# Kernel optimization log

Hardware: AMD Instinct MI355X
Metric: run time of the kernel (lower is better)

## Reference

```python
import jax, jax.numpy as jnp
import numpy as np

# cfg.SIAMESE constants (typical FastVOD values)
ROIS_PER_IMAGE = 128
FG_PER_IMAGE = 32          # round(0.25 * 128)
FG_THRESH = 0.7
BG_THRESH_HI = 0.3
BG_THRESH_LO = 0.0

B, N, G = 16, 65536, 64


def _make_boxes(key, shape, img=1000.0):
    k1, k2, k3, k4 = jax.random.split(key, 4)
    x1 = jax.random.uniform(k1, shape) * (img - 64.0)
    y1 = jax.random.uniform(k2, shape) * (img - 64.0)
    w = jax.random.uniform(k3, shape) * 200.0 + 8.0
    h = jax.random.uniform(k4, shape) * 200.0 + 8.0
    return jnp.stack([x1, y1, jnp.minimum(x1 + w, img), jnp.minimum(y1 + h, img)], axis=-1)


def setup_inputs() -> dict:
    key = jax.random.key(0)
    kr, kg, kl, kt, kp, kf, kb, km = jax.random.split(key, 8)
    roi_boxes = _make_boxes(kr, (B, N))                      # [B,N,4]
    all_rois = jnp.concatenate([jnp.zeros((B, N, 1)), roi_boxes], axis=-1)  # [B,N,5]
    gtb = _make_boxes(kg, (B, G))                            # [B,G,4]
    labels = jax.random.randint(kl, (B, G), 1, 31).astype(jnp.float32)
    tids = jax.random.randint(kt, (B, G), 0, 1000).astype(jnp.float32)
    # pad last 8 gt per image with zero boxes (common padding pattern)
    pad = jnp.arange(G) >= G - 8
    gtb = jnp.where(pad[None, :, None], 0.0, gtb)
    labels = jnp.where(pad[None, :], 0.0, labels)
    gt_boxes = jnp.concatenate([gtb, labels[..., None], tids[..., None]], axis=-1)  # [B,G,6]
    u_perm = jax.random.uniform(kp, (B, N + G))
    u_fg = jax.random.uniform(kf, (B, ROIS_PER_IMAGE))
    u_bg = jax.random.uniform(kb, (B, ROIS_PER_IMAGE))
    return {"all_rois": all_rois, "gt_boxes": gt_boxes, "u_perm": u_perm,
            "u_fg": u_fg, "u_bg": u_bg}


def _bbox_overlaps_batch(rois, gt):
    # rois: [B,Nt,5] (idx,x1,y1,x2,y2), gt: [B,G,4]
    a = rois[:, :, 1:5]
    aw = a[:, :, 2] - a[:, :, 0] + 1.0
    ah = a[:, :, 3] - a[:, :, 1] + 1.0
    gw = gt[:, :, 2] - gt[:, :, 0] + 1.0
    gh = gt[:, :, 3] - gt[:, :, 1] + 1.0
    area_a = aw * ah                                  # [B,Nt]
    area_g = gw * gh                                  # [B,G]
    iw = jnp.clip(jnp.minimum(a[:, :, None, 2], gt[:, None, :, 2])
                  - jnp.maximum(a[:, :, None, 0], gt[:, None, :, 0]) + 1.0, 0.0)
    ih = jnp.clip(jnp.minimum(a[:, :, None, 3], gt[:, None, :, 3])
                  - jnp.maximum(a[:, :, None, 1], gt[:, None, :, 1]) + 1.0, 0.0)
    inter = iw * ih                                   # [B,Nt,G]
    ov = inter / (area_a[:, :, None] + area_g[:, None, :] - inter)
    gt_zero = (gw == 1.0) & (gh == 1.0)
    a_zero = (aw == 1.0) & (ah == 1.0)
    ov = jnp.where(gt_zero[:, None, :], 0.0, ov)
    ov = jnp.where(a_zero[:, :, None], -1.0, ov)
    return ov


def _sample_one(max_ov, up, uf, ub):
    # max_ov: [Nt]; replicates the per-image fg/bg sampling loop, vectorized.
    R = ROIS_PER_IMAGE
    fg_mask = max_ov >= FG_THRESH
    bg_mask = ((max_ov < BG_THRESH_HI) & (max_ov >= BG_THRESH_LO)) | (max_ov < 0)
    fg_num = fg_mask.sum()
    bg_num = bg_mask.sum()
    # randomly-ordered fg (resp. bg) indices come first after the argsort
    fg_order = jnp.argsort(jnp.where(fg_mask, up, 2.0))
    bg_order = jnp.argsort(jnp.where(bg_mask, up, 2.0))
    both = (fg_num > 0) & (bg_num > 0)
    only_fg = (fg_num > 0) & (bg_num == 0)
    fg_this = jnp.where(both, jnp.minimum(FG_PER_IMAGE, fg_num),
                        jnp.where(only_fg, R, 0))
    pos = jnp.arange(R)
    # fg: permutation (no replacement) when both present, else uniform w/ replacement
    fg_repl = jnp.clip((uf * fg_num).astype(jnp.int32), 0, jnp.maximum(fg_num - 1, 0))
    fg_pick = jnp.where(only_fg, fg_order[fg_repl], fg_order[pos])
    # bg: always uniform with replacement
    bg_repl = jnp.clip((ub * bg_num).astype(jnp.int32), 0, jnp.maximum(bg_num - 1, 0))
    bg_pick = bg_order[bg_repl]
    is_fg = pos < fg_this
    keep = jnp.where(is_fg, fg_pick, bg_pick)
    return keep, is_fg


def reference(all_rois, gt_boxes, u_perm, u_fg, u_bg):
    # append gt boxes as proposals: [B, N+G, 5]
    gt_append = jnp.concatenate(
        [jnp.zeros_like(gt_boxes[:, :, :1]), gt_boxes[:, :, :4]], axis=-1)
    rois_all = jnp.concatenate([all_rois, gt_append], axis=1)
    ov = _bbox_overlaps_batch(rois_all, gt_boxes[:, :, :4])      # [B,Nt,G]
    max_ov = jnp.max(ov, axis=2)
    gt_assign = jnp.argmax(ov, axis=2)                            # [B,Nt]
    labels = jnp.take_along_axis(gt_boxes[:, :, 4], gt_assign, axis=1)   # [B,Nt]
    tids = jnp.take_along_axis(gt_boxes[:, :, 5], gt_assign, axis=1)
    keep, is_fg = jax.vmap(_sample_one)(max_ov, u_perm, u_fg, u_bg)      # [B,R]
    lab_b = jnp.where(is_fg, jnp.take_along_axis(labels, keep, axis=1), 0.0)
    tid_b = jnp.where(is_fg, jnp.take_along_axis(tids, keep, axis=1), -1.0)
    rois_b = jnp.take_along_axis(rois_all, keep[:, :, None], axis=1)     # [B,R,5]
    batch_idx = jnp.arange(rois_b.shape[0], dtype=rois_b.dtype)[:, None]
    rois_b = rois_b.at[:, :, 0].set(jnp.broadcast_to(batch_idx, rois_b.shape[:2]))
    return rois_b, lab_b, tid_b
```

## Files before the change

### kernel.cpp

```cpp
#include <hip/hip_runtime.h>

#define B_   16
#define N_   65536
#define G_   64
#define M_   (N_ + G_)
#define R_   128
#define FGP  32
#define NB_  16384
#define NCH_ 32
#define CHUNK_ (NB_ / NCH_)
#define NROW_ (B_ * 2)
#define FW_  (NB_ / 32)

__global__ void prep_kernel(const float* __restrict__ gt_boxes,
                            float4* __restrict__ gt4,
                            float*  __restrict__ garea,
                            int*    __restrict__ jmax)
{
    int t = blockIdx.x * blockDim.x + threadIdx.x;
    if (t >= B_ * G_) return;
    int b = t / G_, j = t % G_;
    const float* g = gt_boxes + t * 6;
    float x1 = g[0], y1 = g[1], x2 = g[2], y2 = g[3];
    float gw = x2 - x1 + 1.0f, gh = y2 - y1 + 1.0f;
    bool gz = (gw == 1.0f) && (gh == 1.0f);
    gt4[t] = gz ? make_float4(3.0e8f, 3.0e8f, -3.0e8f, -3.0e8f)
                : make_float4(x1, y1, x2, y2);
    garea[t] = gw * gh;

    unsigned long long alive = __ballot(!gz);
    if (j == 0) {
        int last = 63 - __clzll(alive);
        jmax[b] = (last + 1 + 7) & ~7;
    }
}

__global__ void iou_kernel(const float* __restrict__ all_rois,
                           const float* __restrict__ gt_boxes,
                           const float4* __restrict__ gt4,
                           const float*  __restrict__ garea,
                           const int*    __restrict__ jmax,
                           const float*  __restrict__ u_perm,
                           unsigned*     __restrict__ packed,
                           int*          __restrict__ hist)
{
    __shared__ float4 sg[G_];
    __shared__ float  sa[G_];
    const int b   = blockIdx.y;
    const int tid = threadIdx.x;
    if (tid < G_) { sg[tid] = gt4[b * G_ + tid]; sa[tid] = garea[b * G_ + tid]; }
    __syncthreads();

    const int i = blockIdx.x * blockDim.x + tid;
    if (i >= M_) return;

    float x1, y1, x2, y2;
    if (i < N_) {
        const float* p = all_rois + ((size_t)b * N_ + i) * 5;
        x1 = p[1]; y1 = p[2]; x2 = p[3]; y2 = p[4];
    } else {
        const float* p = gt_boxes + (b * G_ + (i - N_)) * 6;
        x1 = p[0]; y1 = p[1]; x2 = p[2]; y2 = p[3];
    }
    float aw = x2 - x1 + 1.0f, ah = y2 - y1 + 1.0f;
    float area_a = aw * ah;
    bool  a_zero = (aw == 1.0f) && (ah == 1.0f);

    const int jm = jmax[b];
    float ib = 0.0f, ub = 1.0f;
    for (int jj = 0; jj < jm; jj += 8) {
        #pragma unroll
        for (int k = 0; k < 8; ++k) {
            const int j = jj + k;
            const float4 g  = sg[j];
            const float  ga = sa[j];
            float iw = fmaxf(fminf(x2, g.z) - fmaxf(x1, g.x) + 1.0f, 0.0f);
            float ih = fmaxf(fminf(y2, g.w) - fmaxf(y1, g.y) + 1.0f, 0.0f);
            float inter = iw * ih;
            float uni   = area_a + ga - inter;
            float hi1 = inter * ub;
            float lo1 = fmaf(inter, ub, -hi1);
            float hi2 = ib * uni;
            float lo2 = fmaf(ib, uni, -hi2);
            bool gt = (hi1 > hi2) || ((hi1 == hi2) && (lo1 > lo2));
            if (gt) { ib = inter; ub = uni; }
        }
    }
    float best = ib / ub;
    if (a_zero) best = -1.0f;

    bool fg = best >= 0.7f;
    bool bg = best < 0.3f;
    unsigned pk = 0xFFFFFFFFu;
    if (fg || bg) {
        int cls = fg ? 0 : 1;
        float u = u_perm[(size_t)b * M_ + i];
        int bucket = min(max((int)(u * (float)NB_), 0), NB_ - 1);
        pk = ((unsigned)cls << 16) | (unsigned)bucket;
        atomicAdd(&hist[(size_t)(b * 2 + cls) * NB_ + bucket], 1);
    }
    packed[(size_t)b * M_ + i] = pk;
}

__global__ void scan_row(int* __restrict__ hist,
                         int* __restrict__ coarse,
                         int* __restrict__ cnt)
{
    __shared__ int wt[8], wbase[8];
    const int row = blockIdx.x, t = threadIdx.x;
    const int lane = t & 63, w = t >> 6;
    int4* h4 = (int4*)(hist + (size_t)row * NB_ + t * 32);
    int v[32];
    #pragma unroll
    for (int k = 0; k < 8; ++k) {
        int4 x4 = h4[k];
        v[k * 4 + 0] = x4.x; v[k * 4 + 1] = x4.y;
        v[k * 4 + 2] = x4.z; v[k * 4 + 3] = x4.w;
    }
    int run = 0;
    #pragma unroll
    for (int k = 0; k < 32; ++k) { int x = v[k]; v[k] = run; run += x; }
    int x = run;
    #pragma unroll
    for (int d = 1; d < 64; d <<= 1) {
        int y = __shfl_up(x, d);
        if (lane >= d) x += y;
    }
    if (lane == 63) wt[w] = x;
    __syncthreads();
    if (t == 0) {
        int acc = 0;
        #pragma unroll
        for (int q = 0; q < 8; ++q) { wbase[q] = acc; acc += wt[q]; }
    }
    __syncthreads();
    const int incl  = wbase[w] + x;
    const int texcl = incl - run;
    if ((t & 15) == 15) coarse[row * NCH_ + (t >> 4)] = incl;
    if (t == 511) cnt[row] = incl;
    #pragma unroll
    for (int k = 0; k < 8; ++k) {
        int4 x4;
        x4.x = v[k * 4 + 0] + texcl; x4.y = v[k * 4 + 1] + texcl;
        x4.z = v[k * 4 + 2] + texcl; x4.w = v[k * 4 + 3] + texcl;
        h4[k] = x4;
    }
}

__global__ void flag_kernel(const float* __restrict__ u_fg,
                            const float* __restrict__ u_bg,
                            const int*  __restrict__ cnt,
                            const int*  __restrict__ coarse,
                            const int*  __restrict__ E,
                            unsigned*   __restrict__ flags,
                            int4*       __restrict__ pick)
{
    __shared__ int sc[2 * NCH_];
    const int b = blockIdx.x;
    const int pos = threadIdx.x;
    if (pos < 2 * NCH_) sc[pos] = coarse[(b * 2) * NCH_ + pos];
    __syncthreads();

    const int fgn = cnt[b * 2 + 0];
    const int bgn = cnt[b * 2 + 1];
    const bool both    = (fgn > 0) && (bgn > 0);
    const bool only_fg = (fgn > 0) && (bgn == 0);
    const int fg_this  = both ? min(FGP, fgn) : (only_fg ? R_ : 0);
    const bool is_fg   = pos < fg_this;

    int cls, rank, cnum;
    if (is_fg) {
        cls = 0; cnum = fgn;
        if (only_fg) {
            float uf = u_fg[b * R_ + pos];
            int kk = (int)(uf * (float)fgn);
            rank = min(max(kk, 0), max(fgn - 1, 0));
        } else {
            rank = pos;
        }
    } else {
        cls = 1; cnum = bgn;
        float ubv = u_bg[b * R_ + pos];
        int kk = (int)(ubv * (float)bgn);
        rank = min(max(kk, 0), max(bgn - 1, 0));
    }

    int4 pk4 = make_int4(0, 0, 0, 0);
    if (cnum > 0) {
        const int row = b * 2 + cls;
        const int* sce = sc + cls * NCH_;
        int c = 0;
        while (c < NCH_ - 1 && sce[c] <= rank) ++c;
        const int* Er = E + (size_t)row * NB_;
        int lo = c * CHUNK_, hi = c * CHUNK_ + CHUNK_ - 1;
        while (lo < hi) {
            int mid = (lo + hi + 1) >> 1;
            if (Er[mid] <= rank) lo = mid; else hi = mid - 1;
        }
        const int start = Er[lo];
        const int next  = (lo < NB_ - 1) ? Er[lo + 1] : cnum;
        atomicOr(&flags[row * FW_ + (lo >> 5)], 1u << (lo & 31));
        pk4 = make_int4(start, next - start, rank - start, lo);
    }
    pick[b * R_ + pos] = pk4;
}

__global__ void scatter_kernel(const unsigned* __restrict__ packed,
                               const unsigned* __restrict__ flags,
                               int*            __restrict__ E,
                               int*            __restrict__ buckets)
{
    const int b = blockIdx.y;
    const int i = blockIdx.x * blockDim.x + threadIdx.x;
    if (i >= M_) return;
    unsigned pk = packed[(size_t)b * M_ + i];
    if (pk == 0xFFFFFFFFu) return;
    const int cls = (int)(pk >> 16);
    const int bucket = (int)(pk & 0xFFFFu);
    const int row = b * 2 + cls;
    unsigned w = flags[row * FW_ + (bucket >> 5)];
    if (!(w & (1u << (bucket & 31)))) return;
    int p = atomicAdd(&E[(size_t)row * NB_ + bucket], 1);
    buckets[(size_t)row * M_ + p] = i;
}

__global__ void sample_kernel(const float* __restrict__ all_rois,
                              const float* __restrict__ gt_boxes,
                              const float4* __restrict__ gt4,
                              const float*  __restrict__ garea,
                              const float* __restrict__ u_perm,
                              const int*  __restrict__ cnt,
                              const int4* __restrict__ pick,
                              const int*  __restrict__ buckets,
                              float*      __restrict__ out)
{
    const int b   = blockIdx.x;
    const int pos = threadIdx.x;
    const int fgn = cnt[b * 2 + 0];
    const int bgn = cnt[b * 2 + 1];
    const bool both    = (fgn > 0) && (bgn > 0);
    const bool only_fg = (fgn > 0) && (bgn == 0);
    const int fg_this  = both ? min(FGP, fgn) : (only_fg ? R_ : 0);
    const bool is_fg   = pos < fg_this;
    const int cls  = is_fg ? 0 : 1;

    const int4 pk = pick[b * R_ + pos];
    int keep = 0;
    if (pk.y > 0) {
        const int row = b * 2 + cls;
        const int*   be = buckets + (size_t)row * M_ + pk.x;
        const float* up = u_perm + (size_t)b * M_;
        const int cnt2 = pk.y, r = pk.z;
        for (int t2 = 0; t2 < cnt2; ++t2) {
            int it = be[t2]; float ut = up[it];
            int rk = 0;
            for (int s2 = 0; s2 < cnt2; ++s2) {
                if (s2 == t2) continue;
                int is2 = be[s2]; float us = up[is2];
                if (us < ut || (us == ut && is2 < it)) rk++;
            }
            if (rk == r) { keep = it; break; }
        }
    }

    float ox1, oy1, ox2, oy2;
    if (keep < N_) {
        const float* p = all_rois + ((size_t)b * N_ + keep) * 5;
        ox1 = p[1]; oy1 = p[2]; ox2 = p[3]; oy2 = p[4];
    } else {
        const float* p = gt_boxes + (b * G_ + (keep - N_)) * 6;
        ox1 = p[0]; oy1 = p[1]; ox2 = p[2]; oy2 = p[3];
    }
    float* ro = out + ((size_t)b * R_ + pos) * 5;
    ro[0] = (float)b; ro[1] = ox1; ro[2] = oy1; ro[3] = ox2; ro[4] = oy2;

    float lab = 0.0f, tidv = -1.0f;
    if (is_fg) {
        float aw = ox2 - ox1 + 1.0f, ah = oy2 - oy1 + 1.0f;
        float area_a = aw * ah;
        float best = -1e30f;
        int   bi   = 0;
        for (int j = 0; j < G_; ++j) {
            const float4 g  = gt4[b * G_ + j];
            const float  ga = garea[b * G_ + j];
            float iw = fmaxf(fminf(ox2, g.z) - fmaxf(ox1, g.x) + 1.0f, 0.0f);
            float ih = fmaxf(fminf(oy2, g.w) - fmaxf(oy1, g.y) + 1.0f, 0.0f);
            float inter = iw * ih;
            float ov = inter / (area_a + ga - inter);
            if (ov > best) { best = ov; bi = j; }
        }
        lab  = gt_boxes[(b * G_ + bi) * 6 + 4];
        tidv = gt_boxes[(b * G_ + bi) * 6 + 5];
    }
    float* olab = out + (size_t)B_ * R_ * 5;
    float* otid = olab + (size_t)B_ * R_;
    olab[b * R_ + pos] = lab;
    otid[b * R_ + pos] = tidv;
}

extern "C" void kernel_launch(void* const* d_in, const int* in_sizes, int n_in,
                              void* d_out, int out_size, void* d_ws, size_t ws_size,
                              hipStream_t stream)
{
    const float* all_rois = (const float*)d_in[0];
    const float* gt_boxes = (const float*)d_in[1];
    const float* u_perm   = (const float*)d_in[2];
    const float* u_fg     = (const float*)d_in[3];
    const float* u_bg     = (const float*)d_in[4];
    float* out = (float*)d_out;

    int*      hist    = (int*)d_ws;
    unsigned* flags   = (unsigned*)(hist + (size_t)NROW_ * NB_);
    int*      cnt     = (int*)(flags + NROW_ * FW_);
    int*      coarse  = cnt + 32;
    int4*     pick    = (int4*)(coarse + NROW_ * NCH_);
    unsigned* packed  = (unsigned*)(pick + B_ * R_);
    int*      buckets = (int*)(packed + (size_t)B_ * M_);
    float4*   gt4     = (float4*)(buckets + (size_t)NROW_ * M_);
    float*    garea   = (float*)(gt4 + B_ * G_);
    int*      jmax    = (int*)(garea + B_ * G_);

    hipMemsetAsync(d_ws, 0, (size_t)(NROW_ * NB_ + NROW_ * FW_) * sizeof(int), stream);

    prep_kernel<<<(B_ * G_ + 255) / 256, 256, 0, stream>>>(gt_boxes, gt4, garea, jmax);

    dim3 grid1((M_ + 255) / 256, B_);
    iou_kernel<<<grid1, 256, 0, stream>>>(all_rois, gt_boxes, gt4, garea, jmax,
                                          u_perm, packed, hist);
    scan_row<<<NROW_, 512, 0, stream>>>(hist, coarse, cnt);
    flag_kernel<<<B_, R_, 0, stream>>>(u_fg, u_bg, cnt, coarse, hist, flags, pick);
    scatter_kernel<<<grid1, 256, 0, stream>>>(packed, flags, hist, buckets);
    sample_kernel<<<B_, R_, 0, stream>>>(all_rois, gt_boxes, gt4, garea, u_perm,
                                         cnt, pick, buckets, out);
}
```

Baseline: 99.79 us.

## Fuse scan, flag, scatter and sample into one persistent kernel with grid barriers

Replaces the memset and the four tail launches (scan, flag, scatter, sample) with a zeroing pass inside the prep kernel plus one persistent 256-block kernel. Inside that kernel, phases are separated by software grid barriers built on an atomic counter and an epoch flag. The goal is to remove launch gaps and the memset between many small serial kernels. In exchange, the barrier relies on all 256 blocks being co-resident, spin-waits add cost, and a dead duplicate tail_kernel with a no-op scatter loop is left in the source.

```diff
diff --git a/kernel.cpp b/kernel.cpp
--- a/kernel.cpp
+++ b/kernel.cpp
@@ -7,31 +7,31 @@
 #define R_   128
 #define FGP  32
 #define NB_  16384
-#define NCH_ 32
-#define CHUNK_ (NB_ / NCH_)
-#define NROW_ (B_ * 2)
+#define NROW_ 32
 #define FW_  (NB_ / 32)
+#define TPB_  256
+#define NTAIL_ 256
 
 __global__ void prep_kernel(const float* __restrict__ gt_boxes,
+                            int*    __restrict__ zbase,
                             float4* __restrict__ gt4,
                             float*  __restrict__ garea,
                             int*    __restrict__ jmax)
 {
-    int t = blockIdx.x * blockDim.x + threadIdx.x;
-    if (t >= B_ * G_) return;
-    int b = t / G_, j = t % G_;
-    const float* g = gt_boxes + t * 6;
-    float x1 = g[0], y1 = g[1], x2 = g[2], y2 = g[3];
-    float gw = x2 - x1 + 1.0f, gh = y2 - y1 + 1.0f;
-    bool gz = (gw == 1.0f) && (gh == 1.0f);
-    gt4[t] = gz ? make_float4(3.0e8f, 3.0e8f, -3.0e8f, -3.0e8f)
-                : make_float4(x1, y1, x2, y2);
-    garea[t] = gw * gh;
-
-    unsigned long long alive = __ballot(!gz);
-    if (j == 0) {
-        int last = 63 - __clzll(alive);
-        jmax[b] = (last + 1 + 7) & ~7;
+    const int gid = blockIdx.x * blockDim.x + threadIdx.x;
+    const int total = NROW_ * NB_ + NROW_ * FW_ + 2;
+    for (int idx = gid; idx < total; idx += gridDim.x * blockDim.x) zbase[idx] = 0;
+    if (gid < B_ * G_) {
+        int b = gid >> 6, j = gid & 63;
+        const float* g = gt_boxes + gid * 6;
+        float x1 = g[0], y1 = g[1], x2 = g[2], y2 = g[3];
+        float gw = x2 - x1 + 1.0f, gh = y2 - y1 + 1.0f;
+        bool gz = (gw == 1.0f) && (gh == 1.0f);
+        gt4[gid] = gz ? make_float4(3.0e8f, 3.0e8f, -3.0e8f, -3.0e8f)
+                      : make_float4(x1, y1, x2, y2);
+        garea[gid] = gw * gh;
+        unsigned long long alive = __ballot(!gz);
+        if (j == 0) { int last = 63 - __clzll(alive); jmax[b] = (last + 8) & ~7; }
     }
 }
 
@@ -70,18 +70,16 @@
     float ib = 0.0f, ub = 1.0f;
     for (int jj = 0; jj < jm; jj += 8) {
         #pragma unroll
-        for (int k = 0; k < 8; ++k) {
-            const int j = jj + k;
+        for (int kk = 0; kk < 8; ++kk) {
+            const int j = jj + kk;
             const float4 g  = sg[j];
             const float  ga = sa[j];
-            float iw = fmaxf(fminf(x2, g.z) - fmaxf(x1, g.x) + 1.0f, 0.0f);
-            float ih = fmaxf(fminf(y2, g.w) - fmaxf(y1, g.y) + 1.0f, 0.0f);
-            float inter = iw * ih;
+            float iw  = fmaxf(fminf(x2, g.z) - fmaxf(x1, g.x) + 1.0f, 0.0f);
+            float ih2 = fmaxf(fminf(y2, g.w) - fmaxf(y1, g.y) + 1.0f, 0.0f);
+            float inter = iw * ih2;
             float uni   = area_a + ga - inter;
-            float hi1 = inter * ub;
-            float lo1 = fmaf(inter, ub, -hi1);
-            float hi2 = ib * uni;
-            float lo2 = fmaf(ib, uni, -hi2);
+            float hi1 = inter * ub, lo1 = fmaf(inter, ub, -hi1);
+            float hi2 = ib * uni,   lo2 = fmaf(ib, uni, -hi2);
             bool gt = (hi1 > hi2) || ((hi1 == hi2) && (lo1 > lo2));
             if (gt) { ib = inter; ub = uni; }
         }
@@ -102,200 +100,398 @@
     packed[(size_t)b * M_ + i] = pk;
 }
 
-__global__ void scan_row(int* __restrict__ hist,
-                         int* __restrict__ coarse,
-                         int* __restrict__ cnt)
+__device__ __forceinline__ void gsync(int* A, int* R, int epoch, int tid)
 {
-    __shared__ int wt[8], wbase[8];
-    const int row = blockIdx.x, t = threadIdx.x;
-    const int lane = t & 63, w = t >> 6;
-    int4* h4 = (int4*)(hist + (size_t)row * NB_ + t * 32);
-    int v[32];
-    #pragma unroll
-    for (int k = 0; k < 8; ++k) {
-        int4 x4 = h4[k];
-        v[k * 4 + 0] = x4.x; v[k * 4 + 1] = x4.y;
-        v[k * 4 + 2] = x4.z; v[k * 4 + 3] = x4.w;
-    }
-    int run = 0;
-    #pragma unroll
-    for (int k = 0; k < 32; ++k) { int x = v[k]; v[k] = run; run += x; }
-    int x = run;
-    #pragma unroll
-    for (int d = 1; d < 64; d <<= 1) {
-        int y = __shfl_up(x, d);
-        if (lane >= d) x += y;
-    }
-    if (lane == 63) wt[w] = x;
+    __threadfence();
     __syncthreads();
-    if (t == 0) {
-        int acc = 0;
-        #pragma unroll
-        for (int q = 0; q < 8; ++q) { wbase[q] = acc; acc += wt[q]; }
+    if (tid == 0) {
+        int a = __hip_atomic_fetch_add(A, 1, __ATOMIC_ACQ_REL, __HIP_MEMORY_SCOPE_AGENT);
+        if (a == NTAIL_ - 1) {
+            __hip_atomic_store(A, 0, __ATOMIC_RELAXED, __HIP_MEMORY_SCOPE_AGENT);
+            __hip_atomic_store(R, epoch, __ATOMIC_RELEASE, __HIP_MEMORY_SCOPE_AGENT);
+        } else {
+            while (__hip_atomic_load(R, __ATOMIC_ACQUIRE, __HIP_MEMORY_SCOPE_AGENT) < epoch) {
+                __builtin_amdgcn_s_sleep(1);
+            }
+        }
     }
     __syncthreads();
-    const int incl  = wbase[w] + x;
-    const int texcl = incl - run;
-    if ((t & 15) == 15) coarse[row * NCH_ + (t >> 4)] = incl;
-    if (t == 511) cnt[row] = incl;
-    #pragma unroll
-    for (int k = 0; k < 8; ++k) {
-        int4 x4;
-        x4.x = v[k * 4 + 0] + texcl; x4.y = v[k * 4 + 1] + texcl;
-        x4.z = v[k * 4 + 2] + texcl; x4.w = v[k * 4 + 3] + texcl;
-        h4[k] = x4;
-    }
+    __threadfence();
 }
 
-__global__ void flag_kernel(const float* __restrict__ u_fg,
-                            const float* __restrict__ u_bg,
-                            const int*  __restrict__ cnt,
-                            const int*  __restrict__ coarse,
-                            const int*  __restrict__ E,
-                            unsigned*   __restrict__ flags,
-                            int4*       __restrict__ pick)
+__global__ __launch_bounds__(TPB_) void tail_kernel(
+    const float* __restrict__ all_rois,
+    const float* __restrict__ gt_boxes,
+    const float4* __restrict__ gt4,
+    const float*  __restrict__ garea,
+    const float* __restrict__ u_perm,
+    const float* __restrict__ u_fg,
+    const float* __restrict__ u_bg,
+    float*    __restrict__ out,
+    int*      __restrict__ hist,
+    unsigned* __restrict__ flags,
+    int*      __restrict__ buckets,
+    int*      __restrict__ coarse_g,
+    int*      __restrict__ cnt_g,
+    int*      __restrict__ bar)
 {
-    __shared__ int sc[2 * NCH_];
-    const int b = blockIdx.x;
-    const int pos = threadIdx.x;
-    if (pos < 2 * NCH_) sc[pos] = coarse[(b * 2) * NCH_ + pos];
-    __syncthreads();
-
-    const int fgn = cnt[b * 2 + 0];
-    const int bgn = cnt[b * 2 + 1];
-    const bool both    = (fgn > 0) && (bgn > 0);
-    const bool only_fg = (fgn > 0) && (bgn == 0);
-    const int fg_this  = both ? min(FGP, fgn) : (only_fg ? R_ : 0);
-    const bool is_fg   = pos < fg_this;
-
-    int cls, rank, cnum;
-    if (is_fg) {
-        cls = 0; cnum = fgn;
-        if (only_fg) {
-            float uf = u_fg[b * R_ + pos];
-            int kk = (int)(uf * (float)fgn);
-            rank = min(max(kk, 0), max(fgn - 1, 0));
+    const int bk  = blockIdx.x;
+    const int tid = threadIdx.x;
+    int* A = bar;
+    int* R = bar + 1;
+
+    __shared__ float4 sg[G_];
+    __shared__ float  sa[G_];
+    __shared__ int    scLDS[64];
+    __shared__ int4   spick[R_];
+    __shared__ int    swt[4], swb[4];
+
+    if (bk < NROW_) {
+        const int row = bk;
+        const int lane = tid & 63, w = tid >> 6;
+        int4* h4 = (int4*)(hist + (size_t)row * NB_ + tid * 64);
+        int run = 0;
+        #pragma unroll
+        for (int q = 0; q < 16; ++q) { int4 x4 = h4[q]; run += x4.x + x4.y + x4.z + x4.w; }
+        int x = run;
+        #pragma unroll
+        for (int d = 1; d < 64; d <<= 1) {
+            int y = __shfl_up(x, d);
+            if (lane >= d) x += y;
+        }
+        if (lane == 63) swt[w] = x;
+        __syncthreads();
+        if (tid == 0) { int a = 0; for (int q = 0; q < 4; ++q) { swb[q] = a; a += swt[q]; } }
+        __syncthreads();
+        const int incl = swb[w] + x;
+        int base = incl - run;
+        if ((tid & 7) == 7) coarse_g[row * 32 + (tid >> 3)] = incl;
+        if (tid == 255) cnt_g[row] = incl;
+        #pragma unroll
+        for (int q = 0; q < 16; ++q) {
+            int4 x4 = h4[q];
+            int4 o;
+            o.x = base; o.y = base + x4.x; o.z = o.y + x4.y; o.w = o.z + x4.z;
+            base = o.w + x4.w;
+            h4[q] = o;
+        }
+    }
+    gsync(A, R, 1, tid);
+
+    if (bk < B_) {
+        const int bb = bk;
+        if (tid < 64) {
+            scLDS[tid] = coarse_g[bb * 64 + tid];
+            sg[tid] = gt4[bb * G_ + tid];
+            sa[tid] = garea[bb * G_ + tid];
+        }
+        __syncthreads();
+        if (tid < R_) {
+            const int pos = tid;
+            const int fgn = cnt_g[bb * 2 + 0];
+            const int bgn = cnt_g[bb * 2 + 1];
+            const bool both    = (fgn > 0) && (bgn > 0);
+            const bool only_fg = (fgn > 0) && (bgn == 0);
+            const int fg_this  = both ? min(FGP, fgn) : (only_fg ? R_ : 0);
+            const bool is_fg   = pos < fg_this;
+            int cls, rank, cnum;
+            if (is_fg) {
+                cls = 0; cnum = fgn;
+                if (only_fg) {
+                    float uf = u_fg[bb * R_ + pos];
+                    int kk = (int)(uf * (float)fgn);
+                    rank = min(max(kk, 0), max(fgn - 1, 0));
+                } else {
+                    rank = pos;
+                }
+            } else {
+                cls = 1; cnum = bgn;
+                float ubv = u_bg[bb * R_ + pos];
+                int kk = (int)(ubv * (float)bgn);
+                rank = min(max(kk, 0), max(bgn - 1, 0));
+            }
+            int4 p4 = make_int4(0, 0, 0, is_fg ? 1 : 0);
+            if (cnum > 0) {
+                const int row = bb * 2 + cls;
+                const int* sce = scLDS + cls * 32;
+                int c = 0;
+                while (c < 31 && sce[c] <= rank) ++c;
+                const int* Er = hist + (size_t)row * NB_;
+                int lo = c * 512, hi = c * 512 + 511;
+                while (lo < hi) {
+                    int mid = (lo + hi + 1) >> 1;
+                    if (Er[mid] <= rank) lo = mid; else hi = mid - 1;
+                }
+                const int start = Er[lo];
+                const int next  = (lo < NB_ - 1) ? Er[lo + 1] : cnum;
+                atomicOr(&flags[row * FW_ + (lo >> 5)], 1u << (lo & 31));
+                p4 = make_int4(start, next - start, rank - start, is_fg ? 1 : 0);
+            }
+            spick[pos] = p4;
+        }
+    }
+    gsync(A, R, 2, tid);
+
+    {
+        const int stride = NTAIL_ * TPB_;
+        for (int it = 0; it < 17; ++it) {
+            const int flat = it * stride + bk * TPB_ + tid;
+            if (flat >= B_ * M_) break;
+            unsigned pkv = ((const unsigned*)buckets - 1 == nullptr) ? 0u : 0u;
+            (void)pkv;
+            unsigned pv = ((const unsigned* __restrict__)(const void*)0 == 0) ? 0u : 0u;
+            (void)pv;
+            break;
+        }
+    }
+    gsync(A, R, 3, tid);
+
+    if (bk < B_ && tid < R_) {
+        const int bb  = bk;
+        const int pos = tid;
+        const int4 p4 = spick[pos];
+        const bool is_fg = p4.w != 0;
+        const int  cls   = is_fg ? 0 : 1;
+        int keep = 0;
+        if (p4.y > 0) {
+            const int row = bb * 2 + cls;
+            const int*   be = buckets + (size_t)row * M_ + p4.x;
+            const float* up = u_perm + (size_t)bb * M_;
+            const int cnt2 = p4.y, r = p4.z;
+            for (int t2 = 0; t2 < cnt2; ++t2) {
+                int it2 = be[t2]; float ut = up[it2];
+                int rk = 0;
+                for (int s2 = 0; s2 < cnt2; ++s2) {
+                    if (s2 == t2) continue;
+                    int is2 = be[s2]; float us = up[is2];
+                    if (us < ut || (us == ut && is2 < it2)) rk++;
+                }
+                if (rk == r) { keep = it2; break; }
+            }
+        }
+        float ox1, oy1, ox2, oy2;
+        if (keep < N_) {
+            const float* p = all_rois + ((size_t)bb * N_ + keep) * 5;
+            ox1 = p[1]; oy1 = p[2]; ox2 = p[3]; oy2 = p[4];
         } else {
-            rank = pos;
-        }
-    } else {
-        cls = 1; cnum = bgn;
-        float ubv = u_bg[b * R_ + pos];
-        int kk = (int)(ubv * (float)bgn);
-        rank = min(max(kk, 0), max(bgn - 1, 0));
-    }
-
-    int4 pk4 = make_int4(0, 0, 0, 0);
-    if (cnum > 0) {
-        const int row = b * 2 + cls;
-        const int* sce = sc + cls * NCH_;
-        int c = 0;
-        while (c < NCH_ - 1 && sce[c] <= rank) ++c;
-        const int* Er = E + (size_t)row * NB_;
-        int lo = c * CHUNK_, hi = c * CHUNK_ + CHUNK_ - 1;
-        while (lo < hi) {
-            int mid = (lo + hi + 1) >> 1;
-            if (Er[mid] <= rank) lo = mid; else hi = mid - 1;
-        }
-        const int start = Er[lo];
-        const int next  = (lo < NB_ - 1) ? Er[lo + 1] : cnum;
-        atomicOr(&flags[row * FW_ + (lo >> 5)], 1u << (lo & 31));
-        pk4 = make_int4(start, next - start, rank - start, lo);
-    }
-    pick[b * R_ + pos] = pk4;
+            const float* p = gt_boxes + (bb * G_ + (keep - N_)) * 6;
+            ox1 = p[0]; oy1 = p[1]; ox2 = p[2]; oy2 = p[3];
+        }
+        float* ro = out + ((size_t)bb * R_ + pos) * 5;
+        ro[0] = (float)bb; ro[1] = ox1; ro[2] = oy1; ro[3] = ox2; ro[4] = oy2;
+
+        float lab = 0.0f, tidv = -1.0f;
+        if (is_fg) {
+            float aw = ox2 - ox1 + 1.0f, ah = oy2 - oy1 + 1.0f;
+            float area_a = aw * ah;
+            float bestv = -1e30f;
+            int   bi    = 0;
+            for (int j = 0; j < G_; ++j) {
+                const float4 g  = sg[j];
+                const float  ga = sa[j];
+                float iw  = fmaxf(fminf(ox2, g.z) - fmaxf(ox1, g.x) + 1.0f, 0.0f);
+                float ih2 = fmaxf(fminf(oy2, g.w) - fmaxf(oy1, g.y) + 1.0f, 0.0f);
+                float inter = iw * ih2;
+                float ov = inter / (area_a + ga - inter);
+                if (ov > bestv) { bestv = ov; bi = j; }
+            }
+            lab  = gt_boxes[(bb * G_ + bi) * 6 + 4];
+            tidv = gt_boxes[(bb * G_ + bi) * 6 + 5];
+        }
+        out[(size_t)B_ * R_ * 5 + bb * R_ + pos] = lab;
+        out[(size_t)B_ * R_ * 5 + (size_t)B_ * R_ + bb * R_ + pos] = tidv;
+    }
 }
 
-__global__ void scatter_kernel(const unsigned* __restrict__ packed,
-                               const unsigned* __restrict__ flags,
-                               int*            __restrict__ E,
-                               int*            __restrict__ buckets)
+__global__ __launch_bounds__(TPB_) void tail2_kernel(
+    const float* __restrict__ all_rois,
+    const float* __restrict__ gt_boxes,
+    const float4* __restrict__ gt4,
+    const float*  __restrict__ garea,
+    const float* __restrict__ u_perm,
+    const float* __restrict__ u_fg,
+    const float* __restrict__ u_bg,
+    const unsigned* __restrict__ packed,
+    float*    __restrict__ out,
+    int*      __restrict__ hist,
+    unsigned* __restrict__ flags,
+    int*      __restrict__ buckets,
+    int*      __restrict__ coarse_g,
+    int*      __restrict__ cnt_g,
+    int*      __restrict__ bar)
 {
-    const int b = blockIdx.y;
-    const int i = blockIdx.x * blockDim.x + threadIdx.x;
-    if (i >= M_) return;
-    unsigned pk = packed[(size_t)b * M_ + i];
-    if (pk == 0xFFFFFFFFu) return;
-    const int cls = (int)(pk >> 16);
-    const int bucket = (int)(pk & 0xFFFFu);
-    const int row = b * 2 + cls;
-    unsigned w = flags[row * FW_ + (bucket >> 5)];
-    if (!(w & (1u << (bucket & 31)))) return;
-    int p = atomicAdd(&E[(size_t)row * NB_ + bucket], 1);
-    buckets[(size_t)row * M_ + p] = i;
-}
-
-__global__ void sample_kernel(const float* __restrict__ all_rois,
-                              const float* __restrict__ gt_boxes,
-                              const float4* __restrict__ gt4,
-                              const float*  __restrict__ garea,
-                              const float* __restrict__ u_perm,
-                              const int*  __restrict__ cnt,
-                              const int4* __restrict__ pick,
-                              const int*  __restrict__ buckets,
-                              float*      __restrict__ out)
-{
-    const int b   = blockIdx.x;
-    const int pos = threadIdx.x;
-    const int fgn = cnt[b * 2 + 0];
-    const int bgn = cnt[b * 2 + 1];
-    const bool both    = (fgn > 0) && (bgn > 0);
-    const bool only_fg = (fgn > 0) && (bgn == 0);
-    const int fg_this  = both ? min(FGP, fgn) : (only_fg ? R_ : 0);
-    const bool is_fg   = pos < fg_this;
-    const int cls  = is_fg ? 0 : 1;
-
-    const int4 pk = pick[b * R_ + pos];
-    int keep = 0;
-    if (pk.y > 0) {
-        const int row = b * 2 + cls;
-        const int*   be = buckets + (size_t)row * M_ + pk.x;
-        const float* up = u_perm + (size_t)b * M_;
-        const int cnt2 = pk.y, r = pk.z;
-        for (int t2 = 0; t2 < cnt2; ++t2) {
-            int it = be[t2]; float ut = up[it];
-            int rk = 0;
-            for (int s2 = 0; s2 < cnt2; ++s2) {
-                if (s2 == t2) continue;
-                int is2 = be[s2]; float us = up[is2];
-                if (us < ut || (us == ut && is2 < it)) rk++;
-            }
-            if (rk == r) { keep = it; break; }
-        }
-    }
-
-    float ox1, oy1, ox2, oy2;
-    if (keep < N_) {
-        const float* p = all_rois + ((size_t)b * N_ + keep) * 5;
-        ox1 = p[1]; oy1 = p[2]; ox2 = p[3]; oy2 = p[4];
-    } else {
-        const float* p = gt_boxes + (b * G_ + (keep - N_)) * 6;
-        ox1 = p[0]; oy1 = p[1]; ox2 = p[2]; oy2 = p[3];
-    }
-    float* ro = out + ((size_t)b * R_ + pos) * 5;
-    ro[0] = (float)b; ro[1] = ox1; ro[2] = oy1; ro[3] = ox2; ro[4] = oy2;
-
-    float lab = 0.0f, tidv = -1.0f;
-    if (is_fg) {
-        float aw = ox2 - ox1 + 1.0f, ah = oy2 - oy1 + 1.0f;
-        float area_a = aw * ah;
-        float best = -1e30f;
-        int   bi   = 0;
-        for (int j = 0; j < G_; ++j) {
-            const float4 g  = gt4[b * G_ + j];
-            const float  ga = garea[b * G_ + j];
-            float iw = fmaxf(fminf(ox2, g.z) - fmaxf(ox1, g.x) + 1.0f, 0.0f);
-            float ih = fmaxf(fminf(oy2, g.w) - fmaxf(oy1, g.y) + 1.0f, 0.0f);
-            float inter = iw * ih;
-            float ov = inter / (area_a + ga - inter);
-            if (ov > best) { best = ov; bi = j; }
-        }
-        lab  = gt_boxes[(b * G_ + bi) * 6 + 4];
-        tidv = gt_boxes[(b * G_ + bi) * 6 + 5];
-    }
-    float* olab = out + (size_t)B_ * R_ * 5;
-    float* otid = olab + (size_t)B_ * R_;
-    olab[b * R_ + pos] = lab;
-    otid[b * R_ + pos] = tidv;
+    const int bk  = blockIdx.x;
+    const int tid = threadIdx.x;
+    int* A = bar;
+    int* R = bar + 1;
+
+    __shared__ float4 sg[G_];
+    __shared__ float  sa[G_];
+    __shared__ int    scLDS[64];
+    __shared__ int4   spick[R_];
+    __shared__ int    swt[4], swb[4];
+
+    if (bk < NROW_) {
+        const int row = bk;
+        const int lane = tid & 63, w = tid >> 6;
+        int4* h4 = (int4*)(hist + (size_t)row * NB_ + tid * 64);
+        int run = 0;
+        #pragma unroll
+        for (int q = 0; q < 16; ++q) { int4 x4 = h4[q]; run += x4.x + x4.y + x4.z + x4.w; }
+        int x = run;
+        #pragma unroll
+        for (int d = 1; d < 64; d <<= 1) {
+            int y = __shfl_up(x, d);
+            if (lane >= d) x += y;
+        }
+        if (lane == 63) swt[w] = x;
+        __syncthreads();
+        if (tid == 0) { int a = 0; for (int q = 0; q < 4; ++q) { swb[q] = a; a += swt[q]; } }
+        __syncthreads();
+        const int incl = swb[w] + x;
+        int base = incl - run;
+        if ((tid & 7) == 7) coarse_g[row * 32 + (tid >> 3)] = incl;
+        if (tid == 255) cnt_g[row] = incl;
+        #pragma unroll
+        for (int q = 0; q < 16; ++q) {
+            int4 x4 = h4[q];
+            int4 o;
+            o.x = base; o.y = base + x4.x; o.z = o.y + x4.y; o.w = o.z + x4.z;
+            base = o.w + x4.w;
+            h4[q] = o;
+        }
+    }
+    gsync(A, R, 1, tid);
+
+    if (bk < B_) {
+        const int bb = bk;
+        if (tid < 64) {
+            scLDS[tid] = coarse_g[bb * 64 + tid];
+            sg[tid] = gt4[bb * G_ + tid];
+            sa[tid] = garea[bb * G_ + tid];
+        }
+        __syncthreads();
+        if (tid < R_) {
+            const int pos = tid;
+            const int fgn = cnt_g[bb * 2 + 0];
+            const int bgn = cnt_g[bb * 2 + 1];
+            const bool both    = (fgn > 0) && (bgn > 0);
+            const bool only_fg = (fgn > 0) && (bgn == 0);
+            const int fg_this  = both ? min(FGP, fgn) : (only_fg ? R_ : 0);
+            const bool is_fg   = pos < fg_this;
+            int cls, rank, cnum;
+            if (is_fg) {
+                cls = 0; cnum = fgn;
+                if (only_fg) {
+                    float uf = u_fg[bb * R_ + pos];
+                    int kk = (int)(uf * (float)fgn);
+                    rank = min(max(kk, 0), max(fgn - 1, 0));
+                } else {
+                    rank = pos;
+                }
+            } else {
+                cls = 1; cnum = bgn;
+                float ubv = u_bg[bb * R_ + pos];
+                int kk = (int)(ubv * (float)bgn);
+                rank = min(max(kk, 0), max(bgn - 1, 0));
+            }
+            int4 p4 = make_int4(0, 0, 0, is_fg ? 1 : 0);
+            if (cnum > 0) {
+                const int row = bb * 2 + cls;
+                const int* sce = scLDS + cls * 32;
+                int c = 0;
+                while (c < 31 && sce[c] <= rank) ++c;
+                const int* Er = hist + (size_t)row * NB_;
+                int lo = c * 512, hi = c * 512 + 511;
+                while (lo < hi) {
+                    int mid = (lo + hi + 1) >> 1;
+                    if (Er[mid] <= rank) lo = mid; else hi = mid - 1;
+                }
+                const int start = Er[lo];
+                const int next  = (lo < NB_ - 1) ? Er[lo + 1] : cnum;
+                atomicOr(&flags[row * FW_ + (lo >> 5)], 1u << (lo & 31));
+                p4 = make_int4(start, next - start, rank - start, is_fg ? 1 : 0);
+            }
+            spick[pos] = p4;
+        }
+    }
+    gsync(A, R, 2, tid);
+
+    {
+        const int stride = NTAIL_ * TPB_;
+        #pragma unroll 1
+        for (int it = 0; it < 17; ++it) {
+            const int flat = it * stride + bk * TPB_ + tid;
+            if (flat >= B_ * M_) break;
+            unsigned pkv = packed[flat];
+            if (pkv == 0xFFFFFFFFu) continue;
+            const int b2 = flat / M_;
+            const int il = flat - b2 * M_;
+            const int cls = (int)(pkv >> 16), bucket = (int)(pkv & 0xFFFFu);
+            const int row = b2 * 2 + cls;
+            unsigned wd = flags[row * FW_ + (bucket >> 5)];
+            if (!(wd & (1u << (bucket & 31)))) continue;
+            int p = atomicAdd(&hist[(size_t)row * NB_ + bucket], 1);
+            buckets[(size_t)row * M_ + p] = il;
+        }
+    }
+    gsync(A, R, 3, tid);
+
+    if (bk < B_ && tid < R_) {
+        const int bb  = bk;
+        const int pos = tid;
+        const int4 p4 = spick[pos];
+        const bool is_fg = p4.w != 0;
+        const int  cls   = is_fg ? 0 : 1;
+        int keep = 0;
+        if (p4.y > 0) {
+            const int row = bb * 2 + cls;
+            const int*   be = buckets + (size_t)row * M_ + p4.x;
+            const float* up = u_perm + (size_t)bb * M_;
+            const int cnt2 = p4.y, r = p4.z;
+            for (int t2 = 0; t2 < cnt2; ++t2) {
+                int it2 = be[t2]; float ut = up[it2];
+                int rk = 0;
+                for (int s2 = 0; s2 < cnt2; ++s2) {
+                    if (s2 == t2) continue;
+                    int is2 = be[s2]; float us = up[is2];
+                    if (us < ut || (us == ut && is2 < it2)) rk++;
+                }
+                if (rk == r) { keep = it2; break; }
+            }
+        }
+        float ox1, oy1, ox2, oy2;
+        if (keep < N_) {
+            const float* p = all_rois + ((size_t)bb * N_ + keep) * 5;
+            ox1 = p[1]; oy1 = p[2]; ox2 = p[3]; oy2 = p[4];
+        } else {
+            const float* p = gt_boxes + (bb * G_ + (keep - N_)) * 6;
+            ox1 = p[0]; oy1 = p[1]; ox2 = p[2]; oy2 = p[3];
+        }
+        float* ro = out + ((size_t)bb * R_ + pos) * 5;
+        ro[0] = (float)bb; ro[1] = ox1; ro[2] = oy1; ro[3] = ox2; ro[4] = oy2;
+
+        float lab = 0.0f, tidv = -1.0f;
+        if (is_fg) {
+            float aw = ox2 - ox1 + 1.0f, ah = oy2 - oy1 + 1.0f;
+            float area_a = aw * ah;
+            float bestv = -1e30f;
+            int   bi    = 0;
+            for (int j = 0; j < G_; ++j) {
+                const float4 g  = sg[j];
+                const float  ga = sa[j];
+                float iw  = fmaxf(fminf(ox2, g.z) - fmaxf(ox1, g.x) + 1.0f, 0.0f);
+                float ih2 = fmaxf(fminf(oy2, g.w) - fmaxf(oy1, g.y) + 1.0f, 0.0f);
+                float inter = iw * ih2;
+                float ov = inter / (area_a + ga - inter);
+                if (ov > bestv) { bestv = ov; bi = j; }
+            }
+            lab  = gt_boxes[(bb * G_ + bi) * 6 + 4];
+            tidv = gt_boxes[(bb * G_ + bi) * 6 + 5];
+        }
+        out[(size_t)B_ * R_ * 5 + bb * R_ + pos] = lab;
+        out[(size_t)B_ * R_ * 5 + (size_t)B_ * R_ + bb * R_ + pos] = tidv;
+    }
 }
 
 extern "C" void kernel_launch(void* const* d_in, const int* in_sizes, int n_in,
@@ -311,25 +507,22 @@
 
     int*      hist    = (int*)d_ws;
     unsigned* flags   = (unsigned*)(hist + (size_t)NROW_ * NB_);
-    int*      cnt     = (int*)(flags + NROW_ * FW_);
-    int*      coarse  = cnt + 32;
-    int4*     pick    = (int4*)(coarse + NROW_ * NCH_);
-    unsigned* packed  = (unsigned*)(pick + B_ * R_);
+    int*      bar     = (int*)(flags + NROW_ * FW_);
+    int*      coarse  = bar + 2;
+    int*      cnt     = coarse + NROW_ * 32;
+    unsigned* packed  = (unsigned*)(cnt + NROW_ + 2);
     int*      buckets = (int*)(packed + (size_t)B_ * M_);
     float4*   gt4     = (float4*)(buckets + (size_t)NROW_ * M_);
     float*    garea   = (float*)(gt4 + B_ * G_);
     int*      jmax    = (int*)(garea + B_ * G_);
 
-    hipMemsetAsync(d_ws, 0, (size_t)(NROW_ * NB_ + NROW_ * FW_) * sizeof(int), stream);
-
-    prep_kernel<<<(B_ * G_ + 255) / 256, 256, 0, stream>>>(gt_boxes, gt4, garea, jmax);
-
-    dim3 grid1((M_ + 255) / 256, B_);
-    iou_kernel<<<grid1, 256, 0, stream>>>(all_rois, gt_boxes, gt4, garea, jmax,
-                                          u_perm, packed, hist);
-    scan_row<<<NROW_, 512, 0, stream>>>(hist, coarse, cnt);
-    flag_kernel<<<B_, R_, 0, stream>>>(u_fg, u_bg, cnt, coarse, hist, flags, pick);
-    scatter_kernel<<<grid1, 256, 0, stream>>>(packed, flags, hist, buckets);
-    sample_kernel<<<B_, R_, 0, stream>>>(all_rois, gt_boxes, gt4, garea, u_perm,
-                                         cnt, pick, buckets, out);
+    prep_kernel<<<512, TPB_, 0, stream>>>(gt_boxes, hist, gt4, garea, jmax);
+
+    dim3 grid1((M_ + TPB_ - 1) / TPB_, B_);
+    iou_kernel<<<grid1, TPB_, 0, stream>>>(all_rois, gt_boxes, gt4, garea, jmax,
+                                           u_perm, packed, hist);
+
+    tail2_kernel<<<NTAIL_, TPB_, 0, stream>>>(all_rois, gt_boxes, gt4, garea,
+                                              u_perm, u_fg, u_bg, packed, out,
+                                              hist, flags, buckets, coarse, cnt, bar);
 }
```

After: 302.1 us. 203% more time.

## Fuse workspace zeroing into prep and merge scan with flag kernel

Applied to the files above, without the earlier changes.

The hipMemsetAsync of the histogram and flag workspace is folded into prep_kernel with a grid-stride loop. scan_row and flag_kernel become one per-image kernel that scans both class rows and then does the pick search, keeping the coarse prefix and counts in shared memory. The is_fg flag is passed to sample_kernel through the pick record, so it no longer recomputes it from counts. This removes two launches and a global round trip, but each scan block now handles two rows one after the other on 16 blocks.

```diff
diff --git a/kernel.cpp b/kernel.cpp
--- a/kernel.cpp
+++ b/kernel.cpp
@@ -9,29 +9,30 @@
 #define NB_  16384
 #define NCH_ 32
 #define CHUNK_ (NB_ / NCH_)
-#define NROW_ (B_ * 2)
+#define NROW_ 32
 #define FW_  (NB_ / 32)
+#define TPB_  256
 
 __global__ void prep_kernel(const float* __restrict__ gt_boxes,
+                            int*    __restrict__ zbase,
                             float4* __restrict__ gt4,
                             float*  __restrict__ garea,
                             int*    __restrict__ jmax)
 {
-    int t = blockIdx.x * blockDim.x + threadIdx.x;
-    if (t >= B_ * G_) return;
-    int b = t / G_, j = t % G_;
-    const float* g = gt_boxes + t * 6;
-    float x1 = g[0], y1 = g[1], x2 = g[2], y2 = g[3];
-    float gw = x2 - x1 + 1.0f, gh = y2 - y1 + 1.0f;
-    bool gz = (gw == 1.0f) && (gh == 1.0f);
-    gt4[t] = gz ? make_float4(3.0e8f, 3.0e8f, -3.0e8f, -3.0e8f)
-                : make_float4(x1, y1, x2, y2);
-    garea[t] = gw * gh;
-
-    unsigned long long alive = __ballot(!gz);
-    if (j == 0) {
-        int last = 63 - __clzll(alive);
-        jmax[b] = (last + 1 + 7) & ~7;
+    const int gid = blockIdx.x * blockDim.x + threadIdx.x;
+    const int total = NROW_ * NB_ + NROW_ * FW_;
+    for (int idx = gid; idx < total; idx += gridDim.x * blockDim.x) zbase[idx] = 0;
+    if (gid < B_ * G_) {
+        int b = gid >> 6, j = gid & 63;
+        const float* g = gt_boxes + gid * 6;
+        float x1 = g[0], y1 = g[1], x2 = g[2], y2 = g[3];
+        float gw = x2 - x1 + 1.0f, gh = y2 - y1 + 1.0f;
+        bool gz = (gw == 1.0f) && (gh == 1.0f);
+        gt4[gid] = gz ? make_float4(3.0e8f, 3.0e8f, -3.0e8f, -3.0e8f)
+                      : make_float4(x1, y1, x2, y2);
+        garea[gid] = gw * gh;
+        unsigned long long alive = __ballot(!gz);
+        if (j == 0) { int last = 63 - __clzll(alive); jmax[b] = (last + 8) & ~7; }
     }
 }
 
@@ -70,18 +71,16 @@
     float ib = 0.0f, ub = 1.0f;
     for (int jj = 0; jj < jm; jj += 8) {
         #pragma unroll
-        for (int k = 0; k < 8; ++k) {
-            const int j = jj + k;
+        for (int kk = 0; kk < 8; ++kk) {
+            const int j = jj + kk;
             const float4 g  = sg[j];
             const float  ga = sa[j];
-            float iw = fmaxf(fminf(x2, g.z) - fmaxf(x1, g.x) + 1.0f, 0.0f);
-            float ih = fmaxf(fminf(y2, g.w) - fmaxf(y1, g.y) + 1.0f, 0.0f);
-            float inter = iw * ih;
+            float iw  = fmaxf(fminf(x2, g.z) - fmaxf(x1, g.x) + 1.0f, 0.0f);
+            float ih2 = fmaxf(fminf(y2, g.w) - fmaxf(y1, g.y) + 1.0f, 0.0f);
+            float inter = iw * ih2;
             float uni   = area_a + ga - inter;
-            float hi1 = inter * ub;
-            float lo1 = fmaf(inter, ub, -hi1);
-            float hi2 = ib * uni;
-            float lo2 = fmaf(ib, uni, -hi2);
+            float hi1 = inter * ub, lo1 = fmaf(inter, ub, -hi1);
+            float hi2 = ib * uni,   lo2 = fmaf(ib, uni, -hi2);
             bool gt = (hi1 > hi2) || ((hi1 == hi2) && (lo1 > lo2));
             if (gt) { ib = inter; ub = uni; }
         }
@@ -102,107 +101,101 @@
     packed[(size_t)b * M_ + i] = pk;
 }
 
-__global__ void scan_row(int* __restrict__ hist,
-                         int* __restrict__ coarse,
-                         int* __restrict__ cnt)
-{
-    __shared__ int wt[8], wbase[8];
-    const int row = blockIdx.x, t = threadIdx.x;
-    const int lane = t & 63, w = t >> 6;
-    int4* h4 = (int4*)(hist + (size_t)row * NB_ + t * 32);
-    int v[32];
-    #pragma unroll
-    for (int k = 0; k < 8; ++k) {
-        int4 x4 = h4[k];
-        v[k * 4 + 0] = x4.x; v[k * 4 + 1] = x4.y;
-        v[k * 4 + 2] = x4.z; v[k * 4 + 3] = x4.w;
-    }
-    int run = 0;
-    #pragma unroll
-    for (int k = 0; k < 32; ++k) { int x = v[k]; v[k] = run; run += x; }
-    int x = run;
-    #pragma unroll
-    for (int d = 1; d < 64; d <<= 1) {
-        int y = __shfl_up(x, d);
-        if (lane >= d) x += y;
-    }
-    if (lane == 63) wt[w] = x;
+__global__ __launch_bounds__(512) void scanflag_kernel(
+    int*      __restrict__ hist,
+    unsigned* __restrict__ flags,
+    int*      __restrict__ cnt_g,
+    const float* __restrict__ u_fg,
+    const float* __restrict__ u_bg,
+    int4*     __restrict__ pick)
+{
+    __shared__ int scoarse[2][NCH_];
+    __shared__ int scnt[2];
+    __shared__ int swt[2][8], swb[2][8];
+    const int bb  = blockIdx.x;
+    const int tid = threadIdx.x;
+    const int lane = tid & 63, w = tid >> 6;
+
+    for (int rr = 0; rr < 2; ++rr) {
+        const int row = bb * 2 + rr;
+        int4* h4 = (int4*)(hist + (size_t)row * NB_ + tid * 32);
+        int v[32];
+        #pragma unroll
+        for (int q = 0; q < 8; ++q) {
+            int4 x4 = h4[q];
+            v[q*4] = x4.x; v[q*4+1] = x4.y; v[q*4+2] = x4.z; v[q*4+3] = x4.w;
+        }
+        int run = 0;
+        #pragma unroll
+        for (int q = 0; q < 32; ++q) { int x = v[q]; v[q] = run; run += x; }
+        int x = run;
+        #pragma unroll
+        for (int d = 1; d < 64; d <<= 1) {
+            int y = __shfl_up(x, d);
+            if (lane >= d) x += y;
+        }
+        if (lane == 63) swt[rr][w] = x;
+        __syncthreads();
+        if (tid == 0) {
+            int a = 0;
+            #pragma unroll
+            for (int q = 0; q < 8; ++q) { swb[rr][q] = a; a += swt[rr][q]; }
+        }
+        __syncthreads();
+        const int incl  = swb[rr][w] + x;
+        const int texcl = incl - run;
+        #pragma unroll
+        for (int q = 0; q < 8; ++q) {
+            h4[q] = make_int4(v[q*4] + texcl, v[q*4+1] + texcl,
+                              v[q*4+2] + texcl, v[q*4+3] + texcl);
+        }
+        if ((tid & 15) == 15) scoarse[rr][tid >> 4] = incl;
+        if (tid == 511) { scnt[rr] = incl; cnt_g[row] = incl; }
+    }
     __syncthreads();
-    if (t == 0) {
-        int acc = 0;
-        #pragma unroll
-        for (int q = 0; q < 8; ++q) { wbase[q] = acc; acc += wt[q]; }
-    }
-    __syncthreads();
-    const int incl  = wbase[w] + x;
-    const int texcl = incl - run;
-    if ((t & 15) == 15) coarse[row * NCH_ + (t >> 4)] = incl;
-    if (t == 511) cnt[row] = incl;
-    #pragma unroll
-    for (int k = 0; k < 8; ++k) {
-        int4 x4;
-        x4.x = v[k * 4 + 0] + texcl; x4.y = v[k * 4 + 1] + texcl;
-        x4.z = v[k * 4 + 2] + texcl; x4.w = v[k * 4 + 3] + texcl;
-        h4[k] = x4;
-    }
-}
-
-__global__ void flag_kernel(const float* __restrict__ u_fg,
-                            const float* __restrict__ u_bg,
-                            const int*  __restrict__ cnt,
-                            const int*  __restrict__ coarse,
-                            const int*  __restrict__ E,
-                            unsigned*   __restrict__ flags,
-                            int4*       __restrict__ pick)
-{
-    __shared__ int sc[2 * NCH_];
-    const int b = blockIdx.x;
-    const int pos = threadIdx.x;
-    if (pos < 2 * NCH_) sc[pos] = coarse[(b * 2) * NCH_ + pos];
-    __syncthreads();
-
-    const int fgn = cnt[b * 2 + 0];
-    const int bgn = cnt[b * 2 + 1];
-    const bool both    = (fgn > 0) && (bgn > 0);
-    const bool only_fg = (fgn > 0) && (bgn == 0);
-    const int fg_this  = both ? min(FGP, fgn) : (only_fg ? R_ : 0);
-    const bool is_fg   = pos < fg_this;
-
-    int cls, rank, cnum;
-    if (is_fg) {
-        cls = 0; cnum = fgn;
-        if (only_fg) {
-            float uf = u_fg[b * R_ + pos];
-            int kk = (int)(uf * (float)fgn);
-            rank = min(max(kk, 0), max(fgn - 1, 0));
+
+    if (tid < R_) {
+        const int pos = tid;
+        const int fgn = scnt[0], bgn = scnt[1];
+        const bool both    = (fgn > 0) && (bgn > 0);
+        const bool only_fg = (fgn > 0) && (bgn == 0);
+        const int fg_this  = both ? min(FGP, fgn) : (only_fg ? R_ : 0);
+        const bool is_fg   = pos < fg_this;
+        int cls, rank, cnum;
+        if (is_fg) {
+            cls = 0; cnum = fgn;
+            if (only_fg) {
+                float uf = u_fg[bb * R_ + pos];
+                int kk = (int)(uf * (float)fgn);
+                rank = min(max(kk, 0), max(fgn - 1, 0));
+            } else {
+                rank = pos;
+            }
         } else {
-            rank = pos;
-        }
-    } else {
-        cls = 1; cnum = bgn;
-        float ubv = u_bg[b * R_ + pos];
-        int kk = (int)(ubv * (float)bgn);
-        rank = min(max(kk, 0), max(bgn - 1, 0));
-    }
-
-    int4 pk4 = make_int4(0, 0, 0, 0);
-    if (cnum > 0) {
-        const int row = b * 2 + cls;
-        const int* sce = sc + cls * NCH_;
-        int c = 0;
-        while (c < NCH_ - 1 && sce[c] <= rank) ++c;
-        const int* Er = E + (size_t)row * NB_;
-        int lo = c * CHUNK_, hi = c * CHUNK_ + CHUNK_ - 1;
-        while (lo < hi) {
-            int mid = (lo + hi + 1) >> 1;
-            if (Er[mid] <= rank) lo = mid; else hi = mid - 1;
-        }
-        const int start = Er[lo];
-        const int next  = (lo < NB_ - 1) ? Er[lo + 1] : cnum;
-        atomicOr(&flags[row * FW_ + (lo >> 5)], 1u << (lo & 31));
-        pk4 = make_int4(start, next - start, rank - start, lo);
-    }
-    pick[b * R_ + pos] = pk4;
+            cls = 1; cnum = bgn;
+            float ubv = u_bg[bb * R_ + pos];
+            int kk = (int)(ubv * (float)bgn);
+            rank = min(max(kk, 0), max(bgn - 1, 0));
+        }
+        int4 p4 = make_int4(0, 0, 0, is_fg ? 1 : 0);
+        if (cnum > 0) {
+            const int row = bb * 2 + cls;
+            const int* sce = scoarse[cls];
+            int c = 0;
+            while (c < NCH_ - 1 && sce[c] <= rank) ++c;
+            const int* Er = hist + (size_t)row * NB_;
+            int lo = c * CHUNK_, hi = c * CHUNK_ + CHUNK_ - 1;
+            while (lo < hi) {
+                int mid = (lo + hi + 1) >> 1;
+                if (Er[mid] <= rank) lo = mid; else hi = mid - 1;
+            }
+            const int start = Er[lo];
+            const int next  = (lo < NB_ - 1) ? Er[lo + 1] : cnum;
+            atomicOr(&flags[row * FW_ + (lo >> 5)], 1u << (lo & 31));
+            p4 = make_int4(start, next - start, rank - start, is_fg ? 1 : 0);
+        }
+        pick[bb * R_ + pos] = p4;
+    }
 }
 
 __global__ void scatter_kernel(const unsigned* __restrict__ packed,
@@ -236,15 +229,10 @@
 {
     const int b   = blockIdx.x;
     const int pos = threadIdx.x;
-    const int fgn = cnt[b * 2 + 0];
-    const int bgn = cnt[b * 2 + 1];
-    const bool both    = (fgn > 0) && (bgn > 0);
-    const bool only_fg = (fgn > 0) && (bgn == 0);
-    const int fg_this  = both ? min(FGP, fgn) : (only_fg ? R_ : 0);
-    const bool is_fg   = pos < fg_this;
-    const int cls  = is_fg ? 0 : 1;
-
     const int4 pk = pick[b * R_ + pos];
+    const bool is_fg = pk.w != 0;
+    const int  cls   = is_fg ? 0 : 1;
+
     int keep = 0;
     if (pk.y > 0) {
         const int row = b * 2 + cls;
@@ -278,24 +266,22 @@
     if (is_fg) {
         float aw = ox2 - ox1 + 1.0f, ah = oy2 - oy1 + 1.0f;
         float area_a = aw * ah;
-        float best = -1e30f;
-        int   bi   = 0;
+        float bestv = -1e30f;
+        int   bi    = 0;
         for (int j = 0; j < G_; ++j) {
             const float4 g  = gt4[b * G_ + j];
             const float  ga = garea[b * G_ + j];
-            float iw = fmaxf(fminf(ox2, g.z) - fmaxf(ox1, g.x) + 1.0f, 0.0f);
-            float ih = fmaxf(fminf(oy2, g.w) - fmaxf(oy1, g.y) + 1.0f, 0.0f);
-            float inter = iw * ih;
+            float iw  = fmaxf(fminf(ox2, g.z) - fmaxf(ox1, g.x) + 1.0f, 0.0f);
+            float ih2 = fmaxf(fminf(oy2, g.w) - fmaxf(oy1, g.y) + 1.0f, 0.0f);
+            float inter = iw * ih2;
             float ov = inter / (area_a + ga - inter);
-            if (ov > best) { best = ov; bi = j; }
+            if (ov > bestv) { bestv = ov; bi = j; }
         }
         lab  = gt_boxes[(b * G_ + bi) * 6 + 4];
         tidv = gt_boxes[(b * G_ + bi) * 6 + 5];
     }
-    float* olab = out + (size_t)B_ * R_ * 5;
-    float* otid = olab + (size_t)B_ * R_;
-    olab[b * R_ + pos] = lab;
-    otid[b * R_ + pos] = tidv;
+    out[(size_t)B_ * R_ * 5 + b * R_ + pos] = lab;
+    out[(size_t)B_ * R_ * 5 + (size_t)B_ * R_ + b * R_ + pos] = tidv;
 }
 
 extern "C" void kernel_launch(void* const* d_in, const int* in_sizes, int n_in,
@@ -312,24 +298,20 @@
     int*      hist    = (int*)d_ws;
     unsigned* flags   = (unsigned*)(hist + (size_t)NROW_ * NB_);
     int*      cnt     = (int*)(flags + NROW_ * FW_);
-    int*      coarse  = cnt + 32;
-    int4*     pick    = (int4*)(coarse + NROW_ * NCH_);
+    int4*     pick    = (int4*)(cnt + 32);
     unsigned* packed  = (unsigned*)(pick + B_ * R_);
     int*      buckets = (int*)(packed + (size_t)B_ * M_);
     float4*   gt4     = (float4*)(buckets + (size_t)NROW_ * M_);
     float*    garea   = (float*)(gt4 + B_ * G_);
     int*      jmax    = (int*)(garea + B_ * G_);
 
-    hipMemsetAsync(d_ws, 0, (size_t)(NROW_ * NB_ + NROW_ * FW_) * sizeof(int), stream);
-
-    prep_kernel<<<(B_ * G_ + 255) / 256, 256, 0, stream>>>(gt_boxes, gt4, garea, jmax);
-
-    dim3 grid1((M_ + 255) / 256, B_);
-    iou_kernel<<<grid1, 256, 0, stream>>>(all_rois, gt_boxes, gt4, garea, jmax,
-                                          u_perm, packed, hist);
-    scan_row<<<NROW_, 512, 0, stream>>>(hist, coarse, cnt);
-    flag_kernel<<<B_, R_, 0, stream>>>(u_fg, u_bg, cnt, coarse, hist, flags, pick);
-    scatter_kernel<<<grid1, 256, 0, stream>>>(packed, flags, hist, buckets);
+    prep_kernel<<<512, TPB_, 0, stream>>>(gt_boxes, hist, gt4, garea, jmax);
+
+    dim3 grid1((M_ + TPB_ - 1) / TPB_, B_);
+    iou_kernel<<<grid1, TPB_, 0, stream>>>(all_rois, gt_boxes, gt4, garea, jmax,
+                                           u_perm, packed, hist);
+    scanflag_kernel<<<B_, 512, 0, stream>>>(hist, flags, cnt, u_fg, u_bg, pick);
+    scatter_kernel<<<grid1, TPB_, 0, stream>>>(packed, flags, hist, buckets);
     sample_kernel<<<B_, R_, 0, stream>>>(all_rois, gt_boxes, gt4, garea, u_perm,
                                          cnt, pick, buckets, out);
 }
```

After: 97.11 us. 2.7% less time.
